# Performance work log

Measured on AMD Instinct MI355X. Metric: run time of the kernel, lower is better.

## Reference

```python
import jax, jax.numpy as jnp
import numpy as np

B, N, DIN, H, A = 4096, 32, 256, 128, 32  # batch, n_agents, din, hidden_dim, n_actions
NEG = 9e15


def _linear_params(key, fan_in, fan_out):
    kw, kb = jax.random.split(key)
    bound = 1.0 / np.sqrt(fan_in)
    w = jax.random.uniform(kw, (fan_in, fan_out), jnp.float32, -bound, bound)
    b = jax.random.uniform(kb, (fan_out,), jnp.float32, -bound, bound)
    return w, b


def setup_inputs() -> dict:
    key = jax.random.key(0)
    ks = jax.random.split(key, 12)
    x = jax.random.normal(ks[0], (B, N, DIN), jnp.float32)
    mask = jax.random.randint(ks[1], (B, N, N), 0, 2).astype(jnp.float32)
    enc_w, enc_b = _linear_params(ks[2], DIN, H)
    a1_vw, a1_vb = _linear_params(ks[3], H, H)
    a1_kw, a1_kb = _linear_params(ks[4], H, H)
    a1_qw, a1_qb = _linear_params(ks[5], H, H)
    a1_ow, a1_ob = _linear_params(ks[6], H, H)
    a2_vw, a2_vb = _linear_params(ks[7], H, H)
    a2_kw, a2_kb = _linear_params(ks[8], H, H)
    a2_qw, a2_qb = _linear_params(ks[9], H, H)
    a2_ow, a2_ob = _linear_params(ks[10], H, H)
    q_w, q_b = _linear_params(ks[11], H, A)
    return dict(x=x, mask=mask, enc_w=enc_w, enc_b=enc_b,
                a1_vw=a1_vw, a1_vb=a1_vb, a1_kw=a1_kw, a1_kb=a1_kb,
                a1_qw=a1_qw, a1_qb=a1_qb, a1_ow=a1_ow, a1_ob=a1_ob,
                a2_vw=a2_vw, a2_vb=a2_vb, a2_kw=a2_kw, a2_kb=a2_kb,
                a2_qw=a2_qw, a2_qb=a2_qb, a2_ow=a2_ow, a2_ob=a2_ob,
                q_w=q_w, q_b=q_b)


def _att_block(h, mask, vw, vb, kw, kb, qw, qb, ow, ob):
    # h: [B, N, H]; mask: [B, N, N]
    v = jax.nn.relu(jnp.einsum('bnd,dh->bnh', h, vw) + vb)
    q = jax.nn.relu(jnp.einsum('bnd,dh->bnh', h, qw) + qb)
    k = jax.nn.relu(jnp.einsum('bnd,dh->bnh', h, kw) + kb)
    scores = jnp.einsum('bih,bjh->bij', q, k)               # [B, N, N]
    logits = scores * mask - NEG * (1.0 - mask)
    att = jax.nn.softmax(logits, axis=2)
    out = jnp.einsum('bij,bjh->bih', att, v)
    return jax.nn.relu(jnp.einsum('bnh,ho->bno', out, ow) + ob)


def reference(x, mask, enc_w, enc_b,
              a1_vw, a1_vb, a1_kw, a1_kb, a1_qw, a1_qb, a1_ow, a1_ob,
              a2_vw, a2_vb, a2_kw, a2_kb, a2_qw, a2_qb, a2_ow, a2_ob,
              q_w, q_b):
    h1 = jax.nn.relu(jnp.einsum('bnd,dh->bnh', x, enc_w) + enc_b)
    h2 = _att_block(h1, mask, a1_vw, a1_vb, a1_kw, a1_kb, a1_qw, a1_qb, a1_ow, a1_ob)
    h3 = _att_block(h2, mask, a2_vw, a2_vb, a2_kw, a2_kb, a2_qw, a2_qb, a2_ow, a2_ob)
    q = jnp.einsum('bnh,ha->bna', h3, q_w) + q_b            # [B, N, A]
    return q
```

## Files before the change

### kernel.cpp

```cpp
#include <hip/hip_runtime.h>
#include <hip/hip_bf16.h>

typedef __attribute__((ext_vector_type(8))) short bf16x8;
typedef __attribute__((ext_vector_type(4))) short bf16x4;
typedef __attribute__((ext_vector_type(4))) float f32x4;

#define DEVI static __device__ __forceinline__

constexpr int NAG = 32, DIN = 256, HDIM = 128, ADIM = 32;

constexpr int WS_ENC = 0;
constexpr int WS_H   = 32768;
constexpr int WS_QW  = 32768 + 8 * 16384;
constexpr int WS_TOT = WS_QW + 4096;

constexpr int SH = 136;
constexpr int SV = 40;
constexpr int SA = 40;
constexpr int SX = 264;

constexpr int L_P0 = 0;
constexpr int L_P1 = 8704;
constexpr int L_P2 = 17408;
constexpr int L_PV = 26112;
constexpr int L_TOT = 36352;

DEVI short f2bf(float f) {
  union { float f; unsigned u; } a; a.f = f;
  return (short)((a.u + 0x7fffu + ((a.u >> 16) & 1u)) >> 16);
}

__global__ void prep_weights(const float* __restrict__ enc_w,
                             const float* __restrict__ m0, const float* __restrict__ m1,
                             const float* __restrict__ m2, const float* __restrict__ m3,
                             const float* __restrict__ m4, const float* __restrict__ m5,
                             const float* __restrict__ m6, const float* __restrict__ m7,
                             const float* __restrict__ qw,
                             short* __restrict__ ws)
{
  const int blk = blockIdx.x, tid = threadIdx.x;
  const float* src; int base, NM, nsh, f4;
  if (blk < 32) { src = enc_w; base = WS_ENC; NM = 8; nsh = 7; f4 = blk * 256 + tid; }
  else if (blk < 160) {
    const int m = (blk - 32) >> 4;
    if      (m == 0) src = m0; else if (m == 1) src = m1;
    else if (m == 2) src = m2; else if (m == 3) src = m3;
    else if (m == 4) src = m4; else if (m == 5) src = m5;
    else if (m == 6) src = m6; else             src = m7;
    base = WS_H + (m << 14); NM = 8; nsh = 7; f4 = ((blk - 32) & 15) * 256 + tid;
  } else { src = qw; base = WS_QW; NM = 2; nsh = 5; f4 = (blk - 160) * 256 + tid; }
  const int s = f4 * 4;
  const int row = s >> nsh, col0 = s & ((1 << nsh) - 1);
  const float4 v = *(const float4*)(src + s);
  const int j = row & 7, ks = row >> 5, lhi = ((row >> 3) & 3) * 16;
  const float vv[4] = {v.x, v.y, v.z, v.w};
#pragma unroll
  for (int c = 0; c < 4; ++c) {
    const int col = col0 + c;
    const int mt = col >> 4, lane = lhi + (col & 15);
    ws[base + (((ks * NM + mt) * 64 + lane) << 3) + j] = f2bf(vv[c]);
  }
}

template<int KSTEPS, bool RELU>
DEVI void linearSw4(const short* __restrict__ src, int sstride,
                    const short* __restrict__ wfrag, const float* __restrict__ bias,
                    short* __restrict__ dst,
                    int mg, int lr, int lq, int lane)
{
  f32x4 acc[2][2];
#pragma unroll
  for (int a = 0; a < 2; ++a)
#pragma unroll
    for (int b = 0; b < 2; ++b) acc[a][b] = (f32x4){0.f, 0.f, 0.f, 0.f};

  const bf16x8* wp = (const bf16x8*)wfrag;
#pragma unroll
  for (int ks = 0; ks < KSTEPS; ++ks) {
    bf16x8 hb[2];
#pragma unroll
    for (int b = 0; b < 2; ++b)
      hb[b] = *(const bf16x8*)(src + (b * 16 + lr) * sstride + ks * 32 + lq * 8);
#pragma unroll
    for (int a = 0; a < 2; ++a) {
      const bf16x8 wa = wp[(ks * 8 + mg * 2 + a) * 64 + lane];
#pragma unroll
      for (int b = 0; b < 2; ++b)
        acc[a][b] = __builtin_amdgcn_mfma_f32_16x16x32_bf16(wa, hb[b], acc[a][b], 0, 0, 0);
    }
  }
#pragma unroll
  for (int a = 0; a < 2; ++a) {
    const float4 bv = *(const float4*)(bias + (mg * 2 + a) * 16 + lq * 4);
    const float bb[4] = {bv.x, bv.y, bv.z, bv.w};
#pragma unroll
    for (int b = 0; b < 2; ++b) {
      bf16x4 s;
#pragma unroll
      for (int r = 0; r < 4; ++r) {
        float v = acc[a][b][r] + bb[r];
        if (RELU) v = fmaxf(v, 0.f);
        s[r] = f2bf(v);
      }
      *(bf16x4*)(dst + (b * 16 + lr) * SH + (mg * 2 + a) * 16 + lq * 4) = s;
    }
  }
}

DEVI void qkv_pass4(const short* __restrict__ h,
                    const short* __restrict__ wq, const short* __restrict__ wk,
                    const short* __restrict__ wv,
                    const float* __restrict__ bq, const float* __restrict__ bk,
                    const float* __restrict__ bv,
                    short* __restrict__ Q, short* __restrict__ K, short* __restrict__ V,
                    int mg, int lr, int lq, int lane)
{
  f32x4 qa[2][2], ka[2][2], va[2][2];
#pragma unroll
  for (int a = 0; a < 2; ++a)
#pragma unroll
    for (int b = 0; b < 2; ++b) {
      qa[a][b] = (f32x4){0.f, 0.f, 0.f, 0.f};
      ka[a][b] = (f32x4){0.f, 0.f, 0.f, 0.f};
      va[a][b] = (f32x4){0.f, 0.f, 0.f, 0.f};
    }
  const bf16x8* wpq = (const bf16x8*)wq;
  const bf16x8* wpk = (const bf16x8*)wk;
  const bf16x8* wpv = (const bf16x8*)wv;
#pragma unroll
  for (int ks = 0; ks < 4; ++ks) {
    bf16x8 hf[2];
#pragma unroll
    for (int b = 0; b < 2; ++b)
      hf[b] = *(const bf16x8*)(h + (b * 16 + lr) * SH + ks * 32 + lq * 8);
#pragma unroll
    for (int a = 0; a < 2; ++a) {
      const bf16x8 wqf = wpq[(ks * 8 + mg * 2 + a) * 64 + lane];
      const bf16x8 wkf = wpk[(ks * 8 + mg * 2 + a) * 64 + lane];
      const bf16x8 wvf = wpv[(ks * 8 + mg * 2 + a) * 64 + lane];
#pragma unroll
      for (int b = 0; b < 2; ++b) {
        qa[a][b] = __builtin_amdgcn_mfma_f32_16x16x32_bf16(wqf, hf[b], qa[a][b], 0, 0, 0);
        ka[a][b] = __builtin_amdgcn_mfma_f32_16x16x32_bf16(wkf, hf[b], ka[a][b], 0, 0, 0);
        va[b][a] = __builtin_amdgcn_mfma_f32_16x16x32_bf16(hf[b], wvf, va[b][a], 0, 0, 0);
      }
    }
  }
#pragma unroll
  for (int a = 0; a < 2; ++a) {
    const float4 bq4 = *(const float4*)(bq + (mg * 2 + a) * 16 + lq * 4);
    const float4 bk4 = *(const float4*)(bk + (mg * 2 + a) * 16 + lq * 4);
    const float qb4[4] = {bq4.x, bq4.y, bq4.z, bq4.w};
    const float kb4[4] = {bk4.x, bk4.y, bk4.z, bk4.w};
#pragma unroll
    for (int b = 0; b < 2; ++b) {
      bf16x4 sq, sk;
#pragma unroll
      for (int r = 0; r < 4; ++r) {
        sq[r] = f2bf(fmaxf(qa[a][b][r] + qb4[r], 0.f));
        sk[r] = f2bf(fmaxf(ka[a][b][r] + kb4[r], 0.f));
      }
      const int off = (b * 16 + lr) * SH + (mg * 2 + a) * 16 + lq * 4;
      *(bf16x4*)(Q + off) = sq;
      *(bf16x4*)(K + off) = sk;
    }
  }
#pragma unroll
  for (int a = 0; a < 2; ++a) {
    const float bvv = bv[(mg * 2 + a) * 16 + lr];
#pragma unroll
    for (int b = 0; b < 2; ++b) {
      bf16x4 sv;
#pragma unroll
      for (int r = 0; r < 4; ++r)
        sv[r] = f2bf(fmaxf(va[b][a][r] + bvv, 0.f));
      *(bf16x4*)(V + ((mg * 2 + a) * 16 + lr) * SV + b * 16 + lq * 4) = sv;
    }
  }
}

DEVI void scores_pass4(const short* __restrict__ Q, const short* __restrict__ K,
                       short* __restrict__ AT, const float* __restrict__ mask,
                       int b0, int qt, int lr, int lq)
{
  f32x4 sc[2];
  sc[0] = (f32x4){0.f, 0.f, 0.f, 0.f};
  sc[1] = (f32x4){0.f, 0.f, 0.f, 0.f};
#pragma unroll
  for (int ks = 0; ks < 4; ++ks) {
    const bf16x8 qf = *(const bf16x8*)(Q + (qt * 16 + lr) * SH + ks * 32 + lq * 8);
#pragma unroll
    for (int kt = 0; kt < 2; ++kt) {
      const bf16x8 kf = *(const bf16x8*)(K + (kt * 16 + lr) * SH + ks * 32 + lq * 8);
      sc[kt] = __builtin_amdgcn_mfma_f32_16x16x32_bf16(kf, qf, sc[kt], 0, 0, 0);
    }
  }
  const float* mp = mask + (size_t)b0 * (NAG * NAG) + (qt * 16 + lr) * 32;
  float l[2][4];
  float M = -3.0e38f;
#pragma unroll
  for (int kt = 0; kt < 2; ++kt) {
    const float4 m4 = *(const float4*)(mp + kt * 16 + lq * 4);
    const float mm[4] = {m4.x, m4.y, m4.z, m4.w};
#pragma unroll
    for (int r = 0; r < 4; ++r) {
      const float v = sc[kt][r] * mm[r] - 9e15f * (1.f - mm[r]);
      l[kt][r] = v;
      M = fmaxf(M, v);
    }
  }
  M = fmaxf(M, __shfl_xor(M, 16));
  M = fmaxf(M, __shfl_xor(M, 32));
  float e[2][4], T = 0.f;
#pragma unroll
  for (int kt = 0; kt < 2; ++kt)
#pragma unroll
    for (int r = 0; r < 4; ++r) { e[kt][r] = __expf(l[kt][r] - M); T += e[kt][r]; }
  T += __shfl_xor(T, 16);
  T += __shfl_xor(T, 32);
  const float rT = __frcp_rn(T);
#pragma unroll
  for (int kt = 0; kt < 2; ++kt) {
    bf16x4 s;
#pragma unroll
    for (int r = 0; r < 4; ++r) s[r] = f2bf(e[kt][r] * rT);
    *(bf16x4*)(AT + (qt * 16 + lr) * SA + kt * 16 + lq * 4) = s;
  }
}

DEVI void pv_pass4(const short* __restrict__ V, const short* __restrict__ AT,
                   short* __restrict__ AO, int wave, int lr, int lq)
{
  bf16x8 atf[2];
#pragma unroll
  for (int qt = 0; qt < 2; ++qt)
    atf[qt] = *(const bf16x8*)(AT + (qt * 16 + lr) * SA + lq * 8);
#pragma unroll
  for (int fi = 0; fi < 2; ++fi) {
    const int f2 = wave * 2 + fi;
    const bf16x8 vf = *(const bf16x8*)(V + (f2 * 16 + lr) * SV + lq * 8);
#pragma unroll
    for (int qt = 0; qt < 2; ++qt) {
      const f32x4 p = __builtin_amdgcn_mfma_f32_16x16x32_bf16(
          vf, atf[qt], (f32x4){0.f, 0.f, 0.f, 0.f}, 0, 0, 0);
      bf16x4 s;
#pragma unroll
      for (int r = 0; r < 4; ++r) s[r] = f2bf(p[r]);
      *(bf16x4*)(AO + (qt * 16 + lr) * SH + f2 * 16 + lq * 4) = s;
    }
  }
}

DEVI void att_block4(const short* Rh, short* RQ, short* RK, short* RV,
                     short* RAT, short* RAO, short* Rout,
                     const short* wv, const short* wk, const short* wq, const short* wo,
                     const float* bv, const float* bk, const float* bq, const float* bo,
                     const float* __restrict__ mask, int b0,
                     int wave, int lr, int lq, int lane)
{
  qkv_pass4(Rh, wq, wk, wv, bq, bk, bv, RQ, RK, RV, wave, lr, lq, lane);
  __syncthreads();
  if (wave < 2) scores_pass4(RQ, RK, RAT, mask, b0, wave, lr, lq);
  __syncthreads();
  pv_pass4(RV, RAT, RAO, wave, lr, lq);
  __syncthreads();
  linearSw4<4, true>(RAO, SH, wo, bo, Rout, wave, lr, lq, lane);
  __syncthreads();
}

__global__ __launch_bounds__(256, 4)
void dgn_main(const float* __restrict__ x, const float* __restrict__ mask,
              const float* __restrict__ enc_b,
              const float* __restrict__ b1v, const float* __restrict__ b1k,
              const float* __restrict__ b1q, const float* __restrict__ b1o,
              const float* __restrict__ b2v, const float* __restrict__ b2k,
              const float* __restrict__ b2q, const float* __restrict__ b2o,
              const float* __restrict__ qb,
              const short* __restrict__ wf,
              float* __restrict__ out)
{
  __shared__ __align__(16) char smem[L_TOT];
  short* P0 = (short*)(smem + L_P0);
  short* P1 = (short*)(smem + L_P1);
  short* P2 = (short*)(smem + L_P2);
  short* PV = (short*)(smem + L_PV);
  short* XB = (short*)(smem + L_P1);

  const int tid = threadIdx.x;
  const int wave = tid >> 6, lane = tid & 63;
  const int lr = lane & 15, lq = lane >> 4;
  const int b0 = blockIdx.x;

  {
    const float4* xsrc = (const float4*)(x + (size_t)b0 * NAG * DIN);
#pragma unroll
    for (int it = 0; it < 8; ++it) {
      const int q4 = tid + it * 256;
      const float4 v = xsrc[q4];
      bf16x4 s;
      s[0] = f2bf(v.x); s[1] = f2bf(v.y); s[2] = f2bf(v.z); s[3] = f2bf(v.w);
      *(bf16x4*)(XB + (q4 >> 6) * SX + (q4 & 63) * 4) = s;
    }
  }
  __syncthreads();

  linearSw4<8, true>(XB, SX, wf + WS_ENC, enc_b, P0, wave, lr, lq, lane);
  __syncthreads();

  att_block4(P0, P1, P2, PV, P0, P1, P2,
             wf + WS_H + 0 * 16384, wf + WS_H + 1 * 16384,
             wf + WS_H + 2 * 16384, wf + WS_H + 3 * 16384,
             b1v, b1k, b1q, b1o, mask, b0, wave, lr, lq, lane);

  att_block4(P2, P0, P1, PV, P2, P0, P1,
             wf + WS_H + 4 * 16384, wf + WS_H + 5 * 16384,
             wf + WS_H + 6 * 16384, wf + WS_H + 7 * 16384,
             b2v, b2k, b2q, b2o, mask, b0, wave, lr, lq, lane);

  if (wave < 2) {
    f32x4 ha[2];
    ha[0] = (f32x4){0.f, 0.f, 0.f, 0.f};
    ha[1] = (f32x4){0.f, 0.f, 0.f, 0.f};
    const bf16x8* wp = (const bf16x8*)(wf + WS_QW);
#pragma unroll
    for (int ks = 0; ks < 4; ++ks) {
      const bf16x8 hf = *(const bf16x8*)(P1 + (wave * 16 + lr) * SH + ks * 32 + lq * 8);
#pragma unroll
      for (int a = 0; a < 2; ++a)
        ha[a] = __builtin_amdgcn_mfma_f32_16x16x32_bf16(wp[(ks * 2 + a) * 64 + lane], hf, ha[a], 0, 0, 0);
    }
    float* op = out + ((size_t)b0 * NAG + wave * 16 + lr) * ADIM;
#pragma unroll
    for (int a = 0; a < 2; ++a) {
      const float4 bv4 = *(const float4*)(qb + a * 16 + lq * 4);
      float4 o;
      o.x = ha[a][0] + bv4.x; o.y = ha[a][1] + bv4.y;
      o.z = ha[a][2] + bv4.z; o.w = ha[a][3] + bv4.w;
      *(float4*)(op + a * 16 + lq * 4) = o;
    }
  }
}

extern "C" void kernel_launch(void* const* d_in, const int* in_sizes, int n_in,
                              void* d_out, int out_size, void* d_ws, size_t ws_size,
                              hipStream_t stream)
{
  const float* x     = (const float*)d_in[0];
  const float* mask  = (const float*)d_in[1];
  const float* enc_w = (const float*)d_in[2];
  const float* enc_b = (const float*)d_in[3];
  const float* a1_vw = (const float*)d_in[4];
  const float* a1_vb = (const float*)d_in[5];
  const float* a1_kw = (const float*)d_in[6];
  const float* a1_kb = (const float*)d_in[7];
  const float* a1_qw = (const float*)d_in[8];
  const float* a1_qb = (const float*)d_in[9];
  const float* a1_ow = (const float*)d_in[10];
  const float* a1_ob = (const float*)d_in[11];
  const float* a2_vw = (const float*)d_in[12];
  const float* a2_vb = (const float*)d_in[13];
  const float* a2_kw = (const float*)d_in[14];
  const float* a2_kb = (const float*)d_in[15];
  const float* a2_qw = (const float*)d_in[16];
  const float* a2_qb = (const float*)d_in[17];
  const float* a2_ow = (const float*)d_in[18];
  const float* a2_ob = (const float*)d_in[19];
  const float* q_w   = (const float*)d_in[20];
  const float* q_b   = (const float*)d_in[21];
  short* ws = (short*)d_ws;

  prep_weights<<<164, 256, 0, stream>>>(
      enc_w, a1_vw, a1_kw, a1_qw, a1_ow, a2_vw, a2_kw, a2_qw, a2_ow, q_w, ws);

  dgn_main<<<4096, 256, 0, stream>>>(
      x, mask, enc_b,
      a1_vb, a1_kb, a1_qb, a1_ob,
      a2_vb, a2_kb, a2_qb, a2_ob,
      q_b, ws, (float*)d_out);
}
```

Measured before the change: 290.2 us.

## Prefetch weight fragments, use hardware bf16 packing, hoist mask loads

Three separate changes. The MFMA loops in the linear and QKV passes now load the next weight fragment from global memory before issuing the current MFMAs, a software-pipelining step meant to hide load latency. Manual round-to-nearest bf16 conversion is replaced with the packed cvt_pk_bf16_f32 builtin when it is available, which cuts ALU work in the epilogues. The mask rows are loaded into registers once at kernel start and reused by both attention blocks instead of being read twice; this, like the prefetch, adds register pressure under launch_bounds(256,4).

```diff
diff --git a/kernel.cpp b/kernel.cpp
--- a/kernel.cpp
+++ b/kernel.cpp
@@ -29,6 +29,25 @@
   union { float f; unsigned u; } a; a.f = f;
   return (short)((a.u + 0x7fffu + ((a.u >> 16) & 1u)) >> 16);
 }
+
+#if __has_builtin(__builtin_amdgcn_cvt_pk_bf16_f32)
+typedef __attribute__((ext_vector_type(2))) __bf16 v2bf;
+DEVI bf16x4 pk4(float x0, float x1, float x2, float x3) {
+  union { v2bf v; unsigned u; } lo, hi;
+  lo.v = __builtin_amdgcn_cvt_pk_bf16_f32(x0, x1);
+  hi.v = __builtin_amdgcn_cvt_pk_bf16_f32(x2, x3);
+  bf16x4 r;
+  r[0] = (short)(lo.u & 0xffff); r[1] = (short)(lo.u >> 16);
+  r[2] = (short)(hi.u & 0xffff); r[3] = (short)(hi.u >> 16);
+  return r;
+}
+#else
+DEVI bf16x4 pk4(float x0, float x1, float x2, float x3) {
+  bf16x4 r;
+  r[0] = f2bf(x0); r[1] = f2bf(x1); r[2] = f2bf(x2); r[3] = f2bf(x3);
+  return r;
+}
+#endif
 
 __global__ void prep_weights(const float* __restrict__ enc_w,
                              const float* __restrict__ m0, const float* __restrict__ m1,
@@ -75,34 +94,38 @@
     for (int b = 0; b < 2; ++b) acc[a][b] = (f32x4){0.f, 0.f, 0.f, 0.f};
 
   const bf16x8* wp = (const bf16x8*)wfrag;
-#pragma unroll
-  for (int ks = 0; ks < KSTEPS; ++ks) {
-    bf16x8 hb[2];
+  bf16x8 wc = wp[(mg * 2) * 64 + lane];
+  bf16x8 hb[2];
+#pragma unroll
+  for (int step = 0; step < KSTEPS * 2; ++step) {
+    const int ks = step >> 1, a = step & 1;
+    bf16x8 wn;
+    if (step + 1 < KSTEPS * 2) {
+      const int s2 = step + 1;
+      wn = wp[(((s2 >> 1) * 8) + mg * 2 + (s2 & 1)) * 64 + lane];
+    }
+    if (a == 0) {
+#pragma unroll
+      for (int b = 0; b < 2; ++b)
+        hb[b] = *(const bf16x8*)(src + (b * 16 + lr) * sstride + ks * 32 + lq * 8);
+    }
 #pragma unroll
     for (int b = 0; b < 2; ++b)
-      hb[b] = *(const bf16x8*)(src + (b * 16 + lr) * sstride + ks * 32 + lq * 8);
-#pragma unroll
-    for (int a = 0; a < 2; ++a) {
-      const bf16x8 wa = wp[(ks * 8 + mg * 2 + a) * 64 + lane];
-#pragma unroll
-      for (int b = 0; b < 2; ++b)
-        acc[a][b] = __builtin_amdgcn_mfma_f32_16x16x32_bf16(wa, hb[b], acc[a][b], 0, 0, 0);
-    }
+      acc[a][b] = __builtin_amdgcn_mfma_f32_16x16x32_bf16(wc, hb[b], acc[a][b], 0, 0, 0);
+    if (step + 1 < KSTEPS * 2) wc = wn;
   }
 #pragma unroll
   for (int a = 0; a < 2; ++a) {
     const float4 bv = *(const float4*)(bias + (mg * 2 + a) * 16 + lq * 4);
-    const float bb[4] = {bv.x, bv.y, bv.z, bv.w};
 #pragma unroll
     for (int b = 0; b < 2; ++b) {
-      bf16x4 s;
-#pragma unroll
-      for (int r = 0; r < 4; ++r) {
-        float v = acc[a][b][r] + bb[r];
-        if (RELU) v = fmaxf(v, 0.f);
-        s[r] = f2bf(v);
+      float v0 = acc[a][b][0] + bv.x, v1 = acc[a][b][1] + bv.y;
+      float v2 = acc[a][b][2] + bv.z, v3 = acc[a][b][3] + bv.w;
+      if (RELU) {
+        v0 = fmaxf(v0, 0.f); v1 = fmaxf(v1, 0.f);
+        v2 = fmaxf(v2, 0.f); v3 = fmaxf(v3, 0.f);
       }
-      *(bf16x4*)(dst + (b * 16 + lr) * SH + (mg * 2 + a) * 16 + lq * 4) = s;
+      *(bf16x4*)(dst + (b * 16 + lr) * SH + (mg * 2 + a) * 16 + lq * 4) = pk4(v0, v1, v2, v3);
     }
   }
 }
@@ -127,61 +150,58 @@
   const bf16x8* wpq = (const bf16x8*)wq;
   const bf16x8* wpk = (const bf16x8*)wk;
   const bf16x8* wpv = (const bf16x8*)wv;
-#pragma unroll
-  for (int ks = 0; ks < 4; ++ks) {
-    bf16x8 hf[2];
-#pragma unroll
-    for (int b = 0; b < 2; ++b)
-      hf[b] = *(const bf16x8*)(h + (b * 16 + lr) * SH + ks * 32 + lq * 8);
-#pragma unroll
-    for (int a = 0; a < 2; ++a) {
-      const bf16x8 wqf = wpq[(ks * 8 + mg * 2 + a) * 64 + lane];
-      const bf16x8 wkf = wpk[(ks * 8 + mg * 2 + a) * 64 + lane];
-      const bf16x8 wvf = wpv[(ks * 8 + mg * 2 + a) * 64 + lane];
-#pragma unroll
-      for (int b = 0; b < 2; ++b) {
-        qa[a][b] = __builtin_amdgcn_mfma_f32_16x16x32_bf16(wqf, hf[b], qa[a][b], 0, 0, 0);
-        ka[a][b] = __builtin_amdgcn_mfma_f32_16x16x32_bf16(wkf, hf[b], ka[a][b], 0, 0, 0);
-        va[b][a] = __builtin_amdgcn_mfma_f32_16x16x32_bf16(hf[b], wvf, va[b][a], 0, 0, 0);
-      }
-    }
+  const int i0 = (mg * 2) * 64 + lane;
+  bf16x8 cq = wpq[i0], ck = wpk[i0], cv = wpv[i0];
+  bf16x8 hf[2];
+#pragma unroll
+  for (int step = 0; step < 8; ++step) {
+    const int ks = step >> 1, a = step & 1;
+    bf16x8 nq, nk, nv;
+    if (step < 7) {
+      const int s2 = step + 1;
+      const int idx = (((s2 >> 1) * 8) + mg * 2 + (s2 & 1)) * 64 + lane;
+      nq = wpq[idx]; nk = wpk[idx]; nv = wpv[idx];
+    }
+    if (a == 0) {
+#pragma unroll
+      for (int b = 0; b < 2; ++b)
+        hf[b] = *(const bf16x8*)(h + (b * 16 + lr) * SH + ks * 32 + lq * 8);
+    }
+#pragma unroll
+    for (int b = 0; b < 2; ++b) {
+      qa[a][b] = __builtin_amdgcn_mfma_f32_16x16x32_bf16(cq, hf[b], qa[a][b], 0, 0, 0);
+      ka[a][b] = __builtin_amdgcn_mfma_f32_16x16x32_bf16(ck, hf[b], ka[a][b], 0, 0, 0);
+      va[b][a] = __builtin_amdgcn_mfma_f32_16x16x32_bf16(hf[b], cv, va[b][a], 0, 0, 0);
+    }
+    if (step < 7) { cq = nq; ck = nk; cv = nv; }
   }
 #pragma unroll
   for (int a = 0; a < 2; ++a) {
     const float4 bq4 = *(const float4*)(bq + (mg * 2 + a) * 16 + lq * 4);
     const float4 bk4 = *(const float4*)(bk + (mg * 2 + a) * 16 + lq * 4);
-    const float qb4[4] = {bq4.x, bq4.y, bq4.z, bq4.w};
-    const float kb4[4] = {bk4.x, bk4.y, bk4.z, bk4.w};
 #pragma unroll
     for (int b = 0; b < 2; ++b) {
-      bf16x4 sq, sk;
-#pragma unroll
-      for (int r = 0; r < 4; ++r) {
-        sq[r] = f2bf(fmaxf(qa[a][b][r] + qb4[r], 0.f));
-        sk[r] = f2bf(fmaxf(ka[a][b][r] + kb4[r], 0.f));
-      }
       const int off = (b * 16 + lr) * SH + (mg * 2 + a) * 16 + lq * 4;
-      *(bf16x4*)(Q + off) = sq;
-      *(bf16x4*)(K + off) = sk;
+      *(bf16x4*)(Q + off) = pk4(fmaxf(qa[a][b][0] + bq4.x, 0.f), fmaxf(qa[a][b][1] + bq4.y, 0.f),
+                                fmaxf(qa[a][b][2] + bq4.z, 0.f), fmaxf(qa[a][b][3] + bq4.w, 0.f));
+      *(bf16x4*)(K + off) = pk4(fmaxf(ka[a][b][0] + bk4.x, 0.f), fmaxf(ka[a][b][1] + bk4.y, 0.f),
+                                fmaxf(ka[a][b][2] + bk4.z, 0.f), fmaxf(ka[a][b][3] + bk4.w, 0.f));
     }
   }
 #pragma unroll
   for (int a = 0; a < 2; ++a) {
     const float bvv = bv[(mg * 2 + a) * 16 + lr];
 #pragma unroll
-    for (int b = 0; b < 2; ++b) {
-      bf16x4 sv;
-#pragma unroll
-      for (int r = 0; r < 4; ++r)
-        sv[r] = f2bf(fmaxf(va[b][a][r] + bvv, 0.f));
-      *(bf16x4*)(V + ((mg * 2 + a) * 16 + lr) * SV + b * 16 + lq * 4) = sv;
-    }
+    for (int b = 0; b < 2; ++b)
+      *(bf16x4*)(V + ((mg * 2 + a) * 16 + lr) * SV + b * 16 + lq * 4) =
+          pk4(fmaxf(va[b][a][0] + bvv, 0.f), fmaxf(va[b][a][1] + bvv, 0.f),
+              fmaxf(va[b][a][2] + bvv, 0.f), fmaxf(va[b][a][3] + bvv, 0.f));
   }
 }
 
 DEVI void scores_pass4(const short* __restrict__ Q, const short* __restrict__ K,
-                       short* __restrict__ AT, const float* __restrict__ mask,
-                       int b0, int qt, int lr, int lq)
+                       short* __restrict__ AT, const float4* __restrict__ mpre,
+                       int qt, int lr, int lq)
 {
   f32x4 sc[2];
   sc[0] = (f32x4){0.f, 0.f, 0.f, 0.f};
@@ -195,13 +215,11 @@
       sc[kt] = __builtin_amdgcn_mfma_f32_16x16x32_bf16(kf, qf, sc[kt], 0, 0, 0);
     }
   }
-  const float* mp = mask + (size_t)b0 * (NAG * NAG) + (qt * 16 + lr) * 32;
   float l[2][4];
   float M = -3.0e38f;
 #pragma unroll
   for (int kt = 0; kt < 2; ++kt) {
-    const float4 m4 = *(const float4*)(mp + kt * 16 + lq * 4);
-    const float mm[4] = {m4.x, m4.y, m4.z, m4.w};
+    const float mm[4] = {mpre[kt].x, mpre[kt].y, mpre[kt].z, mpre[kt].w};
 #pragma unroll
     for (int r = 0; r < 4; ++r) {
       const float v = sc[kt][r] * mm[r] - 9e15f * (1.f - mm[r]);
@@ -220,12 +238,9 @@
   T += __shfl_xor(T, 32);
   const float rT = __frcp_rn(T);
 #pragma unroll
-  for (int kt = 0; kt < 2; ++kt) {
-    bf16x4 s;
-#pragma unroll
-    for (int r = 0; r < 4; ++r) s[r] = f2bf(e[kt][r] * rT);
-    *(bf16x4*)(AT + (qt * 16 + lr) * SA + kt * 16 + lq * 4) = s;
-  }
+  for (int kt = 0; kt < 2; ++kt)
+    *(bf16x4*)(AT + (qt * 16 + lr) * SA + kt * 16 + lq * 4) =
+        pk4(e[kt][0] * rT, e[kt][1] * rT, e[kt][2] * rT, e[kt][3] * rT);
 }
 
 DEVI void pv_pass4(const short* __restrict__ V, const short* __restrict__ AT,
@@ -243,10 +258,7 @@
     for (int qt = 0; qt < 2; ++qt) {
       const f32x4 p = __builtin_amdgcn_mfma_f32_16x16x32_bf16(
           vf, atf[qt], (f32x4){0.f, 0.f, 0.f, 0.f}, 0, 0, 0);
-      bf16x4 s;
-#pragma unroll
-      for (int r = 0; r < 4; ++r) s[r] = f2bf(p[r]);
-      *(bf16x4*)(AO + (qt * 16 + lr) * SH + f2 * 16 + lq * 4) = s;
+      *(bf16x4*)(AO + (qt * 16 + lr) * SH + f2 * 16 + lq * 4) = pk4(p[0], p[1], p[2], p[3]);
     }
   }
 }
@@ -255,12 +267,12 @@
                      short* RAT, short* RAO, short* Rout,
                      const short* wv, const short* wk, const short* wq, const short* wo,
                      const float* bv, const float* bk, const float* bq, const float* bo,
-                     const float* __restrict__ mask, int b0,
+                     const float4* __restrict__ mpre,
                      int wave, int lr, int lq, int lane)
 {
   qkv_pass4(Rh, wq, wk, wv, bq, bk, bv, RQ, RK, RV, wave, lr, lq, lane);
   __syncthreads();
-  if (wave < 2) scores_pass4(RQ, RK, RAT, mask, b0, wave, lr, lq);
+  if (wave < 2) scores_pass4(RQ, RK, RAT, mpre, wave, lr, lq);
   __syncthreads();
   pv_pass4(RV, RAT, RAO, wave, lr, lq);
   __syncthreads();
@@ -291,15 +303,20 @@
   const int lr = lane & 15, lq = lane >> 4;
   const int b0 = blockIdx.x;
 
+  float4 mpre[2];
+  if (wave < 2) {
+    const float* mp = mask + (size_t)b0 * (NAG * NAG) + (wave * 16 + lr) * 32;
+    mpre[0] = *(const float4*)(mp + lq * 4);
+    mpre[1] = *(const float4*)(mp + 16 + lq * 4);
+  }
+
   {
     const float4* xsrc = (const float4*)(x + (size_t)b0 * NAG * DIN);
 #pragma unroll
     for (int it = 0; it < 8; ++it) {
       const int q4 = tid + it * 256;
       const float4 v = xsrc[q4];
-      bf16x4 s;
-      s[0] = f2bf(v.x); s[1] = f2bf(v.y); s[2] = f2bf(v.z); s[3] = f2bf(v.w);
-      *(bf16x4*)(XB + (q4 >> 6) * SX + (q4 & 63) * 4) = s;
+      *(bf16x4*)(XB + (q4 >> 6) * SX + (q4 & 63) * 4) = pk4(v.x, v.y, v.z, v.w);
     }
   }
   __syncthreads();
@@ -310,12 +327,12 @@
   att_block4(P0, P1, P2, PV, P0, P1, P2,
              wf + WS_H + 0 * 16384, wf + WS_H + 1 * 16384,
              wf + WS_H + 2 * 16384, wf + WS_H + 3 * 16384,
-             b1v, b1k, b1q, b1o, mask, b0, wave, lr, lq, lane);
+             b1v, b1k, b1q, b1o, mpre, wave, lr, lq, lane);
 
   att_block4(P2, P0, P1, PV, P2, P0, P1,
              wf + WS_H + 4 * 16384, wf + WS_H + 5 * 16384,
              wf + WS_H + 6 * 16384, wf + WS_H + 7 * 16384,
-             b2v, b2k, b2q, b2o, mask, b0, wave, lr, lq, lane);
+             b2v, b2k, b2q, b2o, mpre, wave, lr, lq, lane);
 
   if (wave < 2) {
     f32x4 ha[2];
```

New measurement: 321.3 us. +10.7%, slower.
